# Kernel tuning notes

Measured on AMD Instinct MI355X. Metric: run time of the kernel, lower is better.

## Reference

```python
import jax, jax.numpy as jnp
import numpy as np
import math

B, S, D, H = 2, 2048, 2048, 16
DH = D // H
NEG = -1e9  # finite stand-in for -inf so fully-masked rows stay NaN-free


def setup_inputs() -> dict:
    key = jax.random.key(0)
    ks = jax.random.split(key, 6)
    x = jax.random.normal(ks[0], (B, S, D), dtype=jnp.float32)
    key_padding_mask = jax.random.randint(ks[1], (B, S), 0, 2, dtype=jnp.int32)
    Wqkv_w = jax.random.normal(ks[2], (3 * D, D), dtype=jnp.float32) / math.sqrt(D)
    Wqkv_b = jnp.zeros((3 * D,), dtype=jnp.float32)
    out_w = jax.random.normal(ks[3], (D, D), dtype=jnp.float32) / math.sqrt(D)
    out_b = jnp.zeros((D,), dtype=jnp.float32)
    return {"x": x, "key_padding_mask": key_padding_mask, "Wqkv_w": Wqkv_w,
            "Wqkv_b": Wqkv_b, "out_w": out_w, "out_b": out_b}


def reference(x, key_padding_mask, Wqkv_w, Wqkv_b, out_w, out_b):
    b, s, d = x.shape
    # fused QKV projection (torch Linear: y = x @ W.T + b)
    qkv = (x @ Wqkv_w.T + Wqkv_b).reshape(b, s, 3, H, DH)
    q, k, v = qkv[:, :, 0], qkv[:, :, 1], qkv[:, :, 2]  # each [b, s, H, DH]
    scale = 1.0 / math.sqrt(DH)
    scores = jnp.einsum('bqhd,bkhd->bhqk', q, k) * scale  # [b, H, s, s]
    # additive key-padding bias: -inf where mask == 0 (finite NEG for stability)
    pad_bias = jnp.where(key_padding_mask == 0, NEG, 0.0).astype(x.dtype)[:, None, None, :]
    # causal mask: key index > query index is disallowed
    causal = jnp.where(jnp.arange(s)[None, :] > jnp.arange(s)[:, None], NEG, 0.0).astype(x.dtype)
    p = jax.nn.softmax(scores + pad_bias + causal, axis=-1)
    attn = jnp.einsum('bhqk,bkhd->bqhd', p, v).reshape(b, s, d)
    return attn @ out_w.T + out_b
```

## Files before the change

### kernel.cpp

```cpp
#include <hip/hip_runtime.h>
#include <cstdint>

typedef unsigned short u16;
typedef __attribute__((ext_vector_type(8))) short short8v;
typedef __attribute__((ext_vector_type(8))) unsigned short u16x8;
typedef __attribute__((ext_vector_type(4))) float floatx4;

typedef unsigned int __attribute__((address_space(1))) as1_u32;
typedef unsigned int __attribute__((address_space(3))) as3_u32;

__device__ __forceinline__ u16 f2bf(float f) {
  union { float f; unsigned u; } v; v.f = f;
  unsigned r = v.u + 0x7FFFu + ((v.u >> 16) & 1u);
  return (u16)(r >> 16);
}

__device__ __forceinline__ unsigned cvt_pk_bf16(float lo, float hi) {
  unsigned r;
  asm("v_cvt_pk_bf16_f32 %0, %1, %2" : "=v"(r) : "v"(lo), "v"(hi));
  return r;
}

__device__ __forceinline__ void gload16(void* lds, const void* g) {
  __builtin_amdgcn_global_load_lds((as1_u32*)(uintptr_t)g, (as3_u32*)(uintptr_t)lds, 16, 0, 0);
}

__global__ __launch_bounds__(256) void f2bf_kernel(const float* __restrict__ in,
                                                   u16* __restrict__ out, int n4) {
  int i = blockIdx.x * 256 + threadIdx.x;
  const int stride = gridDim.x * 256;
  for (; i < n4; i += stride) {
    float4 v = ((const float4*)in)[i];
    ushort4 o;
    o.x = f2bf(v.x); o.y = f2bf(v.y); o.z = f2bf(v.z); o.w = f2bf(v.w);
    ((ushort4*)out)[i] = o;
  }
}

template <int OUT_BF16>
__global__ __launch_bounds__(512, 2)
void gemm256(const u16* __restrict__ A, const u16* __restrict__ B,
             const float* __restrict__ bias, void* __restrict__ C,
             int M, int N, int K) {
  __shared__ u16 lds[2][4][8192];
  const int tid = threadIdx.x;
  const int wid = tid >> 6, lane = tid & 63;
  const int wr = wid >> 2, wc = wid & 3;
  const int li = lane & 15, lg = lane >> 4;
  const int brow = blockIdx.y * 256, bcol = blockIdx.x * 256;
  const int NT = K >> 6;

  const int rowL = tid >> 3;
  const int klog = ((((tid & 7) << 4) ^ ((rowL & 7) << 4)) >> 1);
  const u16* aS = A + (size_t)(brow + rowL) * K + klog;
  const u16* bS = B + (size_t)(bcol + rowL) * K + klog;

#define STG(slot, reg, src, hh, kt_)                                            \
  {                                                                             \
    const u16* s_ = (src) + (size_t)((hh) * 128) * K + (kt_) * 64;              \
    gload16((char*)&lds[slot][reg][0] + tid * 16, s_);                          \
    gload16((char*)&lds[slot][reg][0] + 8192 + tid * 16, s_ + (size_t)64 * K);  \
  }

  floatx4 acc[8][4];
#pragma unroll
  for (int m = 0; m < 8; ++m)
#pragma unroll
    for (int n = 0; n < 4; ++n) acc[m][n] = floatx4{0.f, 0.f, 0.f, 0.f};

  const int kx0 = (lg * 16) ^ ((li & 7) << 4);
  const int kx1 = (64 + lg * 16) ^ ((li & 7) << 4);
  const int ar0 = li * 128;
  const int bc0 = ((wc & 1) * 64 + li) * 128;

  STG(0, 0, aS, 0, 0);
  STG(0, 1, aS, 1, 0);
  STG(0, 2, bS, 0, 0);
  STG(0, 3, bS, 1, 0);
  STG(1, 2, bS, 0, 1);
  STG(1, 3, bS, 1, 1);
  asm volatile("s_waitcnt vmcnt(4)" ::: "memory");
  __builtin_amdgcn_s_barrier();

  for (int t = 0; t < NT; ++t) {
    const int cur = t & 1;
    const char* Ab = (const char*)&lds[cur][wr][0];
    const char* Bb = (const char*)&lds[cur][2 + (wc >> 1)][0];

    short8v bf[4][2], af[2][2];
#pragma unroll
    for (int n = 0; n < 4; ++n) {
      bf[n][0] = *(const short8v*)(Bb + bc0 + n * 2048 + kx0);
      bf[n][1] = *(const short8v*)(Bb + bc0 + n * 2048 + kx1);
    }
#pragma unroll
    for (int mm = 0; mm < 2; ++mm) {
      af[mm][0] = *(const short8v*)(Ab + ar0 + mm * 2048 + kx0);
      af[mm][1] = *(const short8v*)(Ab + ar0 + mm * 2048 + kx1);
    }
    if (t + 1 < NT) STG(cur ^ 1, 0, aS, 0, t + 1);
    asm volatile("s_waitcnt lgkmcnt(8)" ::: "memory");
    __builtin_amdgcn_s_barrier();
    asm volatile("s_waitcnt lgkmcnt(0)" ::: "memory");
    __builtin_amdgcn_s_setprio(1);
#pragma unroll
    for (int mm = 0; mm < 2; ++mm)
#pragma unroll
      for (int ks = 0; ks < 2; ++ks)
#pragma unroll
        for (int n = 0; n < 4; ++n)
          acc[mm][n] = __builtin_amdgcn_mfma_f32_16x16x32_bf16(af[mm][ks], bf[n][ks], acc[mm][n], 0, 0, 0);
    __builtin_amdgcn_s_setprio(0);
    __builtin_amdgcn_s_barrier();

#pragma unroll
    for (int ph = 1; ph < 4; ++ph) {
      const int m0 = ph * 2;
      short8v a2[2][2];
#pragma unroll
      for (int mm = 0; mm < 2; ++mm) {
        a2[mm][0] = *(const short8v*)(Ab + ar0 + (m0 + mm) * 2048 + kx0);
        a2[mm][1] = *(const short8v*)(Ab + ar0 + (m0 + mm) * 2048 + kx1);
      }
      if (ph == 1)      { if (t + 1 < NT) STG(cur ^ 1, 1, aS, 1, t + 1); }
      else if (ph == 2) { if (t + 2 < NT) STG(cur, 2, bS, 0, t + 2); }
      else              { if (t + 2 < NT) STG(cur, 3, bS, 1, t + 2); }
      __builtin_amdgcn_s_barrier();
      asm volatile("s_waitcnt lgkmcnt(0)" ::: "memory");
      __builtin_amdgcn_s_setprio(1);
#pragma unroll
      for (int mm = 0; mm < 2; ++mm)
#pragma unroll
        for (int ks = 0; ks < 2; ++ks)
#pragma unroll
          for (int n = 0; n < 4; ++n)
            acc[m0 + mm][n] = __builtin_amdgcn_mfma_f32_16x16x32_bf16(a2[mm][ks], bf[n][ks], acc[m0 + mm][n], 0, 0, 0);
      __builtin_amdgcn_s_setprio(0);
      if (ph == 3) {
        if (t + 2 < NT) asm volatile("s_waitcnt vmcnt(4)" ::: "memory");
        else            asm volatile("s_waitcnt vmcnt(0)" ::: "memory");
      }
      __builtin_amdgcn_s_barrier();
    }
  }
#undef STG

  const int crow0 = brow + wr * 128 + lg * 4;
  const int ccol0 = bcol + wc * 64 + li;
#pragma unroll
  for (int n = 0; n < 4; ++n) {
    const float bv = bias[ccol0 + n * 16];
#pragma unroll
    for (int m = 0; m < 8; ++m) {
#pragma unroll
      for (int j = 0; j < 4; ++j) {
        const float v = acc[m][n][j] + bv;
        const size_t idx = (size_t)(crow0 + m * 16 + j) * N + (ccol0 + n * 16);
        if (OUT_BF16) ((u16*)C)[idx] = f2bf(v);
        else          ((float*)C)[idx] = v;
      }
    }
  }
}

__global__ __launch_bounds__(256)
void transpose_v(const u16* __restrict__ qkv, u16* __restrict__ vt) {
  __shared__ u16 T[64][136];
  const int st = blockIdx.x, bh = blockIdx.y;
  const int b = bh >> 4, h = bh & 15;
  const int tid = threadIdx.x;
  const u16* src = qkv + (size_t)(b * 2048 + st * 64) * 6144 + 4096 + h * 128;
  u16* dst = vt + (size_t)bh * 128 * 2048 + st * 64;
#pragma unroll
  for (int p = 0; p < 4; ++p) {
    const int e = (p * 256 + tid) * 8;
    const int r = e >> 7, c = e & 127;
    *(u16x8*)&T[r][c] = *(const u16x8*)&src[(size_t)r * 6144 + c];
  }
  __syncthreads();
#pragma unroll
  for (int p = 0; p < 4; ++p) {
    const int e = (p * 256 + tid) * 8;
    const int dh = e >> 6, s0 = e & 63;
    u16x8 o;
#pragma unroll
    for (int j = 0; j < 8; ++j) o[j] = T[s0 + j][dh];
    *(u16x8*)&dst[(size_t)dh * 2048 + s0] = o;
  }
}

__global__ __launch_bounds__(256, 2)
void attn_fused(const u16* __restrict__ qkv, const u16* __restrict__ vt,
                const int* __restrict__ kpm, u16* __restrict__ attn_out) {
  constexpr int S = 2048, DQ = 6144;
  __shared__ u16 Kl[2][64 * 128];
  __shared__ u16 Vl[128 * 64];
  __shared__ float mskf[2048];
  __shared__ int s_any;
  const int bx = blockIdx.x, by = blockIdx.y;
  const int qt = ((by >> 4) & 1) ? bx : (15 - bx);
  const int bh = by;
  const int b = bh >> 4, h = bh & 15;
  const int tid = threadIdx.x, wave = tid >> 6, lane = tid & 63;
  const int lg = lane >> 4, li = lane & 15;
  const int qrow0 = qt * 128 + wave * 32;

  const u16* Qb = qkv + (size_t)b * S * DQ + h * 128;
  const u16* Kb = Qb + 2048;
  const u16* Vtb = vt + (size_t)bh * 128 * 2048;
  const int* mrow = kpm + b * S;

  if (tid == 0) s_any = 0;
  __syncthreads();
  {
    int a = 0;
    for (int j = tid; j < 2048; j += 256) {
      const int mv = mrow[j];
      mskf[j] = mv ? 0.f : -1.0e9f;
      if (mv && j <= qt * 128) a = 1;
    }
    if (a) s_any = 1;
  }
  __syncthreads();
  const int anyv = s_any;
  const int nt = anyv ? (2 * qt + 2) : 32;
  const int causalFromW = anyv ? (qrow0 >> 6) : 0;

  short8v qb[2][4];
#pragma unroll
  for (int m = 0; m < 2; ++m) {
    const u16* qp = Qb + (size_t)(qrow0 + m * 16 + li) * DQ + lg * 8;
#pragma unroll
    for (int kk = 0; kk < 4; ++kk) qb[m][kk] = *(const short8v*)(qp + kk * 32);
  }
  asm volatile("s_waitcnt vmcnt(0)" ::: "memory");

  float mM[2], lSum[2];
  floatx4 oa[2][8];
#pragma unroll
  for (int m = 0; m < 2; ++m) {
    mM[m] = -3.0e38f; lSum[m] = 0.f;
#pragma unroll
    for (int n = 0; n < 8; ++n) oa[m][n] = floatx4{0.f, 0.f, 0.f, 0.f};
  }

  const u16* kSrc[4]; const u16* vSrc[4];
#pragma unroll
  for (int i = 0; i < 4; ++i) {
    const int L = i * 4096 + tid * 16;
    const int r = L >> 8;
    const int c = ((L & 255) ^ ((r & 7) << 4)) >> 1;
    kSrc[i] = Kb + (size_t)r * DQ + c;
    const int d = L >> 7;
    const int sv = ((L & 127) ^ ((d & 7) << 4)) >> 1;
    vSrc[i] = Vtb + (size_t)d * 2048 + sv;
  }

#define STAGE_K(buf, kt_)                                                      \
  {                                                                            \
    const int kv0_ = (kt_) * 64;                                               \
    _Pragma("unroll")                                                          \
    for (int i = 0; i < 4; ++i)                                                \
      gload16((char*)Kl + (buf) * 16384 + i * 4096 + tid * 16,                 \
              kSrc[i] + (size_t)kv0_ * DQ);                                    \
  }
#define STAGE_V(kt_)                                                           \
  {                                                                            \
    const int kv0_ = (kt_) * 64;                                               \
    _Pragma("unroll")                                                          \
    for (int i = 0; i < 4; ++i)                                                \
      gload16((char*)Vl + i * 4096 + tid * 16, vSrc[i] + kv0_);                \
  }

  const float scale = 0.08838834764831845f;

  STAGE_K(0, 0);
  STAGE_V(0);

  for (int kt = 0; kt < nt; ++kt) {
    const int cur = kt & 1;
    const int kv0 = kt * 64;
    if (kt + 1 < nt) {
      STAGE_K(cur ^ 1, kt + 1);
      asm volatile("s_waitcnt vmcnt(8)" ::: "memory");
    } else {
      asm volatile("s_waitcnt vmcnt(4)" ::: "memory");
    }
    __builtin_amdgcn_s_barrier();

    const char* Kcur = (const char*)Kl + cur * 16384;

    floatx4 sc[2][4];
#pragma unroll
    for (int n = 0; n < 4; ++n) { sc[0][n] = floatx4{0,0,0,0}; sc[1][n] = floatx4{0,0,0,0}; }
#pragma unroll
    for (int n = 0; n < 4; ++n) {
      const int r = n * 16 + li;
#pragma unroll
      for (int kk = 0; kk < 4; ++kk) {
        const int byteo = (r * 256 + kk * 64 + lg * 16) ^ ((r & 7) << 4);
        const short8v kf = *(const short8v*)(Kcur + byteo);
        sc[0][n] = __builtin_amdgcn_mfma_f32_16x16x32_bf16(kf, qb[0][kk], sc[0][n], 0, 0, 0);
        sc[1][n] = __builtin_amdgcn_mfma_f32_16x16x32_bf16(kf, qb[1][kk], sc[1][n], 0, 0, 0);
      }
    }

    floatx4 pbv[4];
#pragma unroll
    for (int n = 0; n < 4; ++n)
      pbv[n] = *(const floatx4*)&mskf[kv0 + n * 16 + lg * 4];
    const bool cz = (kt >= causalFromW);

    short8v pf[2][2];
#pragma unroll
    for (int m = 0; m < 2; ++m) {
      const int q_l = qrow0 + m * 16 + li;
      float tmax = -3.0e38f;
#pragma unroll
      for (int n = 0; n < 4; ++n)
#pragma unroll
        for (int j = 0; j < 4; ++j) {
          float s = sc[m][n][j] * scale + pbv[n][j];
          if (cz && (kv0 + n * 16 + lg * 4 + j > q_l)) s -= 1.0e9f;
          sc[m][n][j] = s;
          tmax = fmaxf(tmax, s);
        }
      tmax = fmaxf(tmax, __shfl_xor(tmax, 16));
      tmax = fmaxf(tmax, __shfl_xor(tmax, 32));
      const float mnew = fmaxf(mM[m], tmax);
      const float f = __expf(mM[m] - mnew);
      mM[m] = mnew;
      float rs = 0.f;
#pragma unroll
      for (int n = 0; n < 4; ++n)
#pragma unroll
        for (int j = 0; j < 4; ++j) {
          const float e = __expf(sc[m][n][j] - mnew);
          sc[m][n][j] = e; rs += e;
        }
      rs += __shfl_xor(rs, 16);
      rs += __shfl_xor(rs, 32);
      lSum[m] = lSum[m] * f + rs;
#pragma unroll
      for (int n2 = 0; n2 < 8; ++n2) oa[m][n2] *= f;

      unsigned w32[4][2];
#pragma unroll
      for (int n = 0; n < 4; ++n) {
        w32[n][0] = cvt_pk_bf16(sc[m][n][0], sc[m][n][1]);
        w32[n][1] = cvt_pk_bf16(sc[m][n][2], sc[m][n][3]);
      }
      union PF { short8v s; unsigned w[4]; } pfu[2];
#pragma unroll
      for (int kk2 = 0; kk2 < 2; ++kk2) {
#pragma unroll
        for (int hh = 0; hh < 2; ++hh) {
          unsigned u = w32[2 * kk2][hh], v = w32[2 * kk2 + 1][hh];
          asm volatile("v_permlane32_swap_b32 %0, %1" : "+v"(u), "+v"(v));
          asm volatile("v_permlane16_swap_b32 %0, %1" : "+v"(u), "+v"(v));
          pfu[kk2].w[hh] = u;
          pfu[kk2].w[2 + hh] = v;
        }
      }
      pf[m][0] = pfu[0].s;
      pf[m][1] = pfu[1].s;
    }

    if (kt + 1 < nt) asm volatile("s_waitcnt vmcnt(4)" ::: "memory");
    else             asm volatile("s_waitcnt vmcnt(0)" ::: "memory");
    __builtin_amdgcn_s_barrier();

#pragma unroll
    for (int kk2 = 0; kk2 < 2; ++kk2) {
#pragma unroll
      for (int n2 = 0; n2 < 8; ++n2) {
        const int d = n2 * 16 + li;
        const int vbyte = (d * 128 + kk2 * 64 + lg * 16) ^ ((d & 7) << 4);
        const short8v vf = *(const short8v*)((const char*)Vl + vbyte);
        oa[0][n2] = __builtin_amdgcn_mfma_f32_16x16x32_bf16(vf, pf[0][kk2], oa[0][n2], 0, 0, 0);
        oa[1][n2] = __builtin_amdgcn_mfma_f32_16x16x32_bf16(vf, pf[1][kk2], oa[1][n2], 0, 0, 0);
      }
    }
    __builtin_amdgcn_s_barrier();
    if (kt + 1 < nt) STAGE_V(kt + 1);
  }

  {
    char* Ol = (char*)Kl + wave * 8192;
#pragma unroll
    for (int m = 0; m < 2; ++m) {
      const float inv = 1.0f / lSum[m];
      const int q_ = m * 16 + li;
#pragma unroll
      for (int n2 = 0; n2 < 8; ++n2) {
        unsigned lo = cvt_pk_bf16(oa[m][n2][0] * inv, oa[m][n2][1] * inv);
        unsigned hi = cvt_pk_bf16(oa[m][n2][2] * inv, oa[m][n2][3] * inv);
        const int byteo = (q_ * 256 + n2 * 32 + lg * 8) ^ ((q_ & 7) << 4);
        uint2 pr; pr.x = lo; pr.y = hi;
        *(uint2*)(Ol + byteo) = pr;
      }
    }
    asm volatile("s_waitcnt lgkmcnt(0)" ::: "memory");
#pragma unroll
    for (int rr = 0; rr < 4; ++rr) {
      const int r = rr * 8 + (lane >> 3);
      const size_t grow = (size_t)(b * 2048 + qt * 128 + wave * 32 + r) * 2048 + h * 128;
#pragma unroll
      for (int s2 = 0; s2 < 2; ++s2) {
        const int byteo = (r * 256 + (lane & 7) * 32 + s2 * 16) ^ ((r & 7) << 4);
        const u16x8 val = *(const u16x8*)(Ol + byteo);
        *(u16x8*)&attn_out[grow + (lane & 7) * 16 + s2 * 8] = val;
      }
    }
  }
#undef STAGE_K
#undef STAGE_V
}

extern "C" void kernel_launch(void* const* d_in, const int* in_sizes, int n_in,
                              void* d_out, int out_size, void* d_ws, size_t ws_size,
                              hipStream_t stream) {
  const float* x    = (const float*)d_in[0];
  const int*   kpm  = (const int*)d_in[1];
  const float* wqkv = (const float*)d_in[2];
  const float* bqkv = (const float*)d_in[3];
  const float* wout = (const float*)d_in[4];
  const float* bout = (const float*)d_in[5];
  float* out = (float*)d_out;

  char* ws = (char*)d_ws;
  u16* xbf   = (u16*)(ws);
  u16* wqbf  = (u16*)(ws + (16u << 20));
  u16* wobf  = (u16*)(ws + (40u << 20));
  u16* qkvb  = (u16*)(ws + (48u << 20));
  u16* vtb   = (u16*)(ws + (96u << 20));
  u16* attnb = (u16*)(ws + (112u << 20));

  f2bf_kernel<<<1024, 256, 0, stream>>>(x,    xbf,  4096 * 2048 / 4);
  f2bf_kernel<<<1024, 256, 0, stream>>>(wqkv, wqbf, 6144 * 2048 / 4);
  f2bf_kernel<<<1024, 256, 0, stream>>>(wout, wobf, 2048 * 2048 / 4);

  gemm256<1><<<dim3(24, 16), 512, 0, stream>>>(xbf, wqbf, bqkv, qkvb, 4096, 6144, 2048);
  transpose_v<<<dim3(32, 32), 256, 0, stream>>>(qkvb, vtb);
  attn_fused<<<dim3(16, 32), 256, 0, stream>>>(qkvb, vtb, kpm, attnb);
  gemm256<0><<<dim3(8, 16), 512, 0, stream>>>(attnb, wobf, bout, out, 4096, 2048, 2048);
}
```

Baseline: 315.5 us.

## Shrink GEMM tile to 128x256 and add XCD-aware 1D block swizzle

Replaces the 256x256 GEMM tile with a 128x256 tile, halving the A staging and accumulator footprint and collapsing the four-phase inner loop into two phases. Launches on a 1D grid with a block-index swizzle that groups blocks across XCDs for L2 reuse. This doubles block counts so the output projection fills all CUs and the wave quantization improves, at the cost of lower arithmetic intensity per tile.

```diff
diff --git a/kernel.cpp b/kernel.cpp
--- a/kernel.cpp
+++ b/kernel.cpp
@@ -39,15 +39,21 @@
 
 template <int OUT_BF16>
 __global__ __launch_bounds__(512, 2)
-void gemm256(const u16* __restrict__ A, const u16* __restrict__ B,
-             const float* __restrict__ bias, void* __restrict__ C,
-             int M, int N, int K) {
-  __shared__ u16 lds[2][4][8192];
+void gemm_bt2(const u16* __restrict__ A, const u16* __restrict__ B,
+              const float* __restrict__ bias, void* __restrict__ C,
+              int M, int N, int K) {
+  __shared__ u16 Al[2][128 * 64];
+  __shared__ u16 Bl[2][256 * 64];
   const int tid = threadIdx.x;
   const int wid = tid >> 6, lane = tid & 63;
   const int wr = wid >> 2, wc = wid & 3;
   const int li = lane & 15, lg = lane >> 4;
-  const int brow = blockIdx.y * 256, bcol = blockIdx.x * 256;
+  const int nwg = gridDim.x;
+  const int bid = blockIdx.x;
+  const int swz = (bid & 7) * (nwg >> 3) + (bid >> 3);
+  const int mcnt = M >> 7;
+  const int bm = swz % mcnt, bn = swz / mcnt;
+  const int brow = bm * 128, bcol = bn * 256;
   const int NT = K >> 6;
 
   const int rowL = tid >> 3;
@@ -55,37 +61,42 @@
   const u16* aS = A + (size_t)(brow + rowL) * K + klog;
   const u16* bS = B + (size_t)(bcol + rowL) * K + klog;
 
-#define STG(slot, reg, src, hh, kt_)                                            \
+#define STG_A(slot, kt_)                                                        \
   {                                                                             \
-    const u16* s_ = (src) + (size_t)((hh) * 128) * K + (kt_) * 64;              \
-    gload16((char*)&lds[slot][reg][0] + tid * 16, s_);                          \
-    gload16((char*)&lds[slot][reg][0] + 8192 + tid * 16, s_ + (size_t)64 * K);  \
-  }
-
-  floatx4 acc[8][4];
-#pragma unroll
-  for (int m = 0; m < 8; ++m)
+    const u16* s_ = aS + (kt_) * 64;                                            \
+    gload16((char*)&Al[slot][0] + tid * 16, s_);                                \
+    gload16((char*)&Al[slot][0] + 8192 + tid * 16, s_ + (size_t)64 * K);        \
+  }
+#define STG_B(slot, kt_)                                                        \
+  {                                                                             \
+    const u16* s_ = bS + (kt_) * 64;                                            \
+    _Pragma("unroll")                                                           \
+    for (int c_ = 0; c_ < 4; ++c_)                                              \
+      gload16((char*)&Bl[slot][0] + c_ * 8192 + tid * 16,                       \
+              s_ + (size_t)(c_ * 64) * K);                                      \
+  }
+
+  floatx4 acc[4][4];
+#pragma unroll
+  for (int m = 0; m < 4; ++m)
 #pragma unroll
     for (int n = 0; n < 4; ++n) acc[m][n] = floatx4{0.f, 0.f, 0.f, 0.f};
 
   const int kx0 = (lg * 16) ^ ((li & 7) << 4);
   const int kx1 = (64 + lg * 16) ^ ((li & 7) << 4);
-  const int ar0 = li * 128;
-  const int bc0 = ((wc & 1) * 64 + li) * 128;
-
-  STG(0, 0, aS, 0, 0);
-  STG(0, 1, aS, 1, 0);
-  STG(0, 2, bS, 0, 0);
-  STG(0, 3, bS, 1, 0);
-  STG(1, 2, bS, 0, 1);
-  STG(1, 3, bS, 1, 1);
+  const int ar0 = (wr * 64 + li) * 128;
+  const int bc0 = (wc * 64 + li) * 128;
+
+  STG_A(0, 0);
+  STG_B(0, 0);
+  STG_B(1, 1);
   asm volatile("s_waitcnt vmcnt(4)" ::: "memory");
   __builtin_amdgcn_s_barrier();
 
   for (int t = 0; t < NT; ++t) {
     const int cur = t & 1;
-    const char* Ab = (const char*)&lds[cur][wr][0];
-    const char* Bb = (const char*)&lds[cur][2 + (wc >> 1)][0];
+    const char* Ab = (const char*)&Al[cur][0];
+    const char* Bb = (const char*)&Bl[cur][0];
 
     short8v bf[4][2], af[2][2];
 #pragma unroll
@@ -98,7 +109,7 @@
       af[mm][0] = *(const short8v*)(Ab + ar0 + mm * 2048 + kx0);
       af[mm][1] = *(const short8v*)(Ab + ar0 + mm * 2048 + kx1);
     }
-    if (t + 1 < NT) STG(cur ^ 1, 0, aS, 0, t + 1);
+    if (t + 1 < NT) STG_A(cur ^ 1, t + 1);
     asm volatile("s_waitcnt lgkmcnt(8)" ::: "memory");
     __builtin_amdgcn_s_barrier();
     asm volatile("s_waitcnt lgkmcnt(0)" ::: "memory");
@@ -113,45 +124,38 @@
     __builtin_amdgcn_s_setprio(0);
     __builtin_amdgcn_s_barrier();
 
-#pragma unroll
-    for (int ph = 1; ph < 4; ++ph) {
-      const int m0 = ph * 2;
-      short8v a2[2][2];
-#pragma unroll
-      for (int mm = 0; mm < 2; ++mm) {
-        a2[mm][0] = *(const short8v*)(Ab + ar0 + (m0 + mm) * 2048 + kx0);
-        a2[mm][1] = *(const short8v*)(Ab + ar0 + (m0 + mm) * 2048 + kx1);
-      }
-      if (ph == 1)      { if (t + 1 < NT) STG(cur ^ 1, 1, aS, 1, t + 1); }
-      else if (ph == 2) { if (t + 2 < NT) STG(cur, 2, bS, 0, t + 2); }
-      else              { if (t + 2 < NT) STG(cur, 3, bS, 1, t + 2); }
-      __builtin_amdgcn_s_barrier();
-      asm volatile("s_waitcnt lgkmcnt(0)" ::: "memory");
-      __builtin_amdgcn_s_setprio(1);
-#pragma unroll
-      for (int mm = 0; mm < 2; ++mm)
-#pragma unroll
-        for (int ks = 0; ks < 2; ++ks)
-#pragma unroll
-          for (int n = 0; n < 4; ++n)
-            acc[m0 + mm][n] = __builtin_amdgcn_mfma_f32_16x16x32_bf16(a2[mm][ks], bf[n][ks], acc[m0 + mm][n], 0, 0, 0);
-      __builtin_amdgcn_s_setprio(0);
-      if (ph == 3) {
-        if (t + 2 < NT) asm volatile("s_waitcnt vmcnt(4)" ::: "memory");
-        else            asm volatile("s_waitcnt vmcnt(0)" ::: "memory");
-      }
-      __builtin_amdgcn_s_barrier();
-    }
-  }
-#undef STG
-
-  const int crow0 = brow + wr * 128 + lg * 4;
+    short8v a2[2][2];
+#pragma unroll
+    for (int mm = 0; mm < 2; ++mm) {
+      a2[mm][0] = *(const short8v*)(Ab + ar0 + (2 + mm) * 2048 + kx0);
+      a2[mm][1] = *(const short8v*)(Ab + ar0 + (2 + mm) * 2048 + kx1);
+    }
+    if (t + 2 < NT) STG_B(cur, t + 2);
+    __builtin_amdgcn_s_barrier();
+    asm volatile("s_waitcnt lgkmcnt(0)" ::: "memory");
+    __builtin_amdgcn_s_setprio(1);
+#pragma unroll
+    for (int mm = 0; mm < 2; ++mm)
+#pragma unroll
+      for (int ks = 0; ks < 2; ++ks)
+#pragma unroll
+        for (int n = 0; n < 4; ++n)
+          acc[2 + mm][n] = __builtin_amdgcn_mfma_f32_16x16x32_bf16(a2[mm][ks], bf[n][ks], acc[2 + mm][n], 0, 0, 0);
+    __builtin_amdgcn_s_setprio(0);
+    if (t + 2 < NT) asm volatile("s_waitcnt vmcnt(4)" ::: "memory");
+    else            asm volatile("s_waitcnt vmcnt(0)" ::: "memory");
+    __builtin_amdgcn_s_barrier();
+  }
+#undef STG_A
+#undef STG_B
+
+  const int crow0 = brow + wr * 64 + lg * 4;
   const int ccol0 = bcol + wc * 64 + li;
 #pragma unroll
   for (int n = 0; n < 4; ++n) {
     const float bv = bias[ccol0 + n * 16];
 #pragma unroll
-    for (int m = 0; m < 8; ++m) {
+    for (int m = 0; m < 4; ++m) {
 #pragma unroll
       for (int j = 0; j < 4; ++j) {
         const float v = acc[m][n][j] + bv;
@@ -440,8 +444,8 @@
   f2bf_kernel<<<1024, 256, 0, stream>>>(wqkv, wqbf, 6144 * 2048 / 4);
   f2bf_kernel<<<1024, 256, 0, stream>>>(wout, wobf, 2048 * 2048 / 4);
 
-  gemm256<1><<<dim3(24, 16), 512, 0, stream>>>(xbf, wqbf, bqkv, qkvb, 4096, 6144, 2048);
+  gemm_bt2<1><<<768, 512, 0, stream>>>(xbf, wqbf, bqkv, qkvb, 4096, 6144, 2048);
   transpose_v<<<dim3(32, 32), 256, 0, stream>>>(qkvb, vtb);
   attn_fused<<<dim3(16, 32), 256, 0, stream>>>(qkvb, vtb, kpm, attnb);
-  gemm256<0><<<dim3(8, 16), 512, 0, stream>>>(attnb, wobf, bout, out, 4096, 2048, 2048);
-}
+  gemm_bt2<0><<<256, 512, 0, stream>>>(attnb, wobf, bout, out, 4096, 2048, 2048);
+}
```

Result: faster. 290.6 us (-7.9%).
